# Performance work log

Measured on AMD Instinct MI355X. Metric: run time of the kernel, lower is better.

## Reference

```python
import jax, jax.numpy as jnp
import numpy as np

T, C, I, E = 8192, 512, 64, 32
NEG = -float(jnp.finfo(jnp.bfloat16).max)  # matches -torch.finfo(bfloat16).max in source


def _l2norm(x, axis):
    return x / jnp.maximum(jnp.linalg.norm(x, axis=axis, keepdims=True), 1e-12)


def setup_inputs() -> dict:
    key = jax.random.key(0)
    k1, k2, k3, k4 = jax.random.split(key, 4)
    hidden_states = jax.random.normal(k1, (T, C), dtype=jnp.float32)
    sim_matrix = jax.random.normal(k2, (C, E), dtype=jnp.float32)
    gates = jnp.zeros((E,), dtype=jnp.float32)
    # nn.Linear default init ~ U(-1/sqrt(fan_in), 1/sqrt(fan_in)); any scale works for a reference
    W1 = jax.random.uniform(k3, (E, C, I), dtype=jnp.float32, minval=-1, maxval=1) / np.sqrt(C)
    W2 = jax.random.uniform(k4, (E, I, C), dtype=jnp.float32, minval=-1, maxval=1) / np.sqrt(I)
    return {"hidden_states": hidden_states, "sim_matrix": sim_matrix, "gates": gates, "W1": W1, "W2": W2}


def reference(hidden_states, sim_matrix, gates, W1, W2):
    x = hidden_states
    # --- DynamicGate ---
    logits = _l2norm(x, -1) @ _l2norm(sim_matrix, 0)          # (T, E) cosine similarity
    pre_act_logits = logits - jax.nn.sigmoid(gates)            # (T, E)
    gated = jax.nn.relu(pre_act_logits)
    # STE: forward hard 0/1, backward identity
    ste_mask = gated + jax.lax.stop_gradient((gated > 0).astype(gated.dtype) - gated)
    inactive = jnp.sum(ste_mask > 0, axis=1) == 0              # tokens with no active expert
    k_fb = E // 2
    _, topk_idx = jax.lax.top_k(logits, k_fb)                  # (T, k_fb)
    onehot = jnp.zeros((T, E), dtype=bool).at[jnp.arange(T)[:, None], topk_idx].set(True)
    fb_pos = inactive[:, None] & onehot                        # positions force-set to 1.0
    activation_mask = jnp.where(fb_pos, jnp.float32(1.0), ste_mask)
    masked = jnp.where(activation_mask > 0, gated, NEG)
    routing_weights = jax.nn.softmax(masked, axis=-1)          # (T, E)
    # --- experts (dense equivalent of sort-dispatch; inactive pairs are zeroed,
    # matching the (T,E,C) zero tensor + index_put_ in the source) ---
    h = jax.nn.gelu(jnp.einsum('tc,eci->tei', x, W1), approximate=False)
    y = jnp.einsum('tei,eic->tec', h, W2)                      # (T, E, C)
    full_expert_outputs = y * jax.lax.stop_gradient(activation_mask)[:, :, None]
    final_output = jnp.einsum('te,tec->tc', routing_weights, full_expert_outputs)
    return final_output, full_expert_outputs, pre_act_logits, activation_mask
```

## Files before the change

kernel.cpp:

```cpp
#include <hip/hip_runtime.h>
#include <math.h>

#define T_ 8192
#define C_ 512
#define I_ 64
#define E_ 32

static constexpr float NEGMAX = -3.3895313892515355e+38f;

typedef float v4f __attribute__((ext_vector_type(4)));

static constexpr size_t WS_RW       = 0;
static constexpr size_t WS_SIMNORM  = (size_t)T_ * E_;
static constexpr size_t WS_MASKBITS = WS_SIMNORM + 64;
static constexpr size_t WS_ACOUNT   = WS_MASKBITS + T_;
static constexpr size_t WS_ALIST    = WS_ACOUNT + 64;

static constexpr size_t OUT_FINAL = 0;
static constexpr size_t OUT_FEO   = (size_t)T_ * C_;
static constexpr size_t OUT_PAL   = OUT_FEO + (size_t)T_ * E_ * C_;
static constexpr size_t OUT_AM    = OUT_PAL + (size_t)T_ * E_;

__global__ __launch_bounds__(256) void k_simnorm(const float* __restrict__ sim,
                                                 double* __restrict__ simnorm) {
  int e = threadIdx.x & 31, seg = threadIdx.x >> 5;
  double s = 0.0;
  for (int c = seg * 64; c < seg * 64 + 64; ++c) {
    double v = (double)sim[(size_t)c * E_ + e];
    s = fma(v, v, s);
  }
  __shared__ double red[8][32];
  red[seg][e] = s;
  __syncthreads();
  if (threadIdx.x < 32) {
    double tot = 0.0;
    for (int k = 0; k < 8; ++k) tot += red[k][threadIdx.x];
    simnorm[threadIdx.x] = sqrt(tot);
  }
}

__global__ __launch_bounds__(256) void k_gate(
    const float* __restrict__ x, const float* __restrict__ sim,
    const float* __restrict__ gates, const double* __restrict__ simnorm,
    float* __restrict__ pal, float* __restrict__ am,
    float* __restrict__ rw, unsigned* __restrict__ maskbits) {
  int lane = threadIdx.x & 63, wv = threadIdx.x >> 6;
  int t = blockIdx.x * 4 + wv;

  __shared__ float xr[4][512];
  const float* xp = x + (size_t)t * C_;
  v4f v0 = *(const v4f*)(xp + lane * 8);
  v4f v1 = *(const v4f*)(xp + lane * 8 + 4);
  *(v4f*)&xr[wv][lane * 8] = v0;
  *(v4f*)&xr[wv][lane * 8 + 4] = v1;
  double ss = (double)v0[0]*v0[0] + (double)v0[1]*v0[1]
            + (double)v0[2]*v0[2] + (double)v0[3]*v0[3]
            + (double)v1[0]*v1[0] + (double)v1[1]*v1[1]
            + (double)v1[2]*v1[2] + (double)v1[3]*v1[3];
  #pragma unroll
  for (int m = 1; m < 64; m <<= 1) ss += __shfl_xor(ss, m, 64);
  __syncthreads();

  int h = lane >> 5, e = lane & 31;
  const float* sp = sim + (size_t)(h * 256) * E_ + e;
  const float* xh = &xr[wv][h * 256];
  double acc = 0.0;
  #pragma unroll 8
  for (int c = 0; c < 256; ++c)
    acc = fma((double)xh[c], (double)sp[(size_t)c * E_], acc);
  acc += __shfl_xor(acc, 32, 64);

  double xn = sqrt(ss); if (xn < 1e-12) xn = 1e-12;
  double sn = simnorm[e]; if (sn < 1e-12) sn = 1e-12;
  float logit = (float)(acc / (xn * sn));
  float sg  = 1.f / (1.f + expf(-gates[e]));
  float pre = logit - sg;
  float gated = fmaxf(pre, 0.f);
  bool act = gated > 0.f;

  unsigned long long bal = __ballot(act);
  bool tok_inactive = ((unsigned)(bal & 0xffffffffull) == 0u);

  float mask;
  if (tok_inactive) {
    int rank = 0;
    #pragma unroll 1
    for (int j2 = 0; j2 < 32; ++j2) {
      float lj = __shfl(logit, j2, 32);
      if (lj > logit || (lj == logit && j2 < e)) ++rank;
    }
    mask = (rank < 16) ? 1.f : 0.f;
  } else {
    mask = act ? 1.f : 0.f;
  }

  float masked = (mask > 0.f) ? gated : NEGMAX;
  float mx = masked;
  #pragma unroll
  for (int m = 1; m < 32; m <<= 1) mx = fmaxf(mx, __shfl_xor(mx, m, 32));
  float ex = expf(masked - mx);
  float sum = ex;
  #pragma unroll
  for (int m = 1; m < 32; m <<= 1) sum += __shfl_xor(sum, m, 32);
  float w = ex / sum;

  unsigned mb = (unsigned)(__ballot(mask > 0.f) & 0xffffffffull);
  if (h == 0) {
    pal[(size_t)t * E_ + e] = pre;
    am [(size_t)t * E_ + e] = mask;
    rw [(size_t)t * E_ + e] = w;
    if (e == 0) maskbits[t] = mb;
  }
}

__global__ __launch_bounds__(1024) void k_lists(const unsigned* __restrict__ maskbits,
                                                unsigned* __restrict__ acount,
                                                unsigned* __restrict__ alist) {
  int e = blockIdx.x;
  int tid = threadIdx.x, lane = tid & 63, wv = tid >> 6;
  __shared__ unsigned wcnt[16], woff[16], stotal, sbase;
  if (tid == 0) sbase = 0;
  __syncthreads();
  for (int chunk = 0; chunk < 8; ++chunk) {
    int t = chunk * 1024 + tid;
    bool bit = (maskbits[t] >> e) & 1u;
    unsigned long long bal = __ballot(bit);
    unsigned prefix = (unsigned)__popcll(bal & ((1ull << lane) - 1ull));
    if (lane == 0) wcnt[wv] = (unsigned)__popcll(bal);
    __syncthreads();
    if (tid == 0) {
      unsigned r = 0;
      for (int k = 0; k < 16; ++k) { woff[k] = r; r += wcnt[k]; }
      stotal = r;
    }
    __syncthreads();
    if (bit) alist[(size_t)e * T_ + sbase + woff[wv] + prefix] = (unsigned)t;
    __syncthreads();
    if (tid == 0) sbase += stotal;
    __syncthreads();
  }
  if (tid == 0) acount[e] = sbase;
}

__global__ __launch_bounds__(256) void k_expert(
    const float* __restrict__ x, const float* __restrict__ W1,
    const float* __restrict__ W2, const unsigned* __restrict__ acount,
    const unsigned* __restrict__ alist, float* __restrict__ feo) {
  int bid = blockIdx.x;
  int xcd = bid & 7, j = bid >> 3;
  int e = xcd + 8 * (j & 3);
  int chunk = j >> 2;
  unsigned nact = acount[e];
  int start = chunk * 64;
  if ((unsigned)start >= nact) return;
  int nt = min(64, (int)nact - start);

  __shared__ __align__(16) char arena[51200];
  float (*xT)[68] = (float (*)[68])arena;
  float* w1t      = (float*)(arena + 17408);
  float* w2p      = (float*)arena;
  float (*hT)[68] = (float (*)[68])(arena + 33792);
  __shared__ int toks[64];

  int tid = threadIdx.x;
  if (tid < 64) {
    int idx = start + tid;
    toks[tid] = (int)alist[(size_t)e * T_ + ((idx < (int)nact) ? idx : start)];
  }
  __syncthreads();

  int ty = tid >> 4, tx = tid & 15;
  int tl = tid >> 2, m = tid & 3;
  const float* xrow = x + (size_t)toks[tl] * C_;

  float acc1[4][4];
  #pragma unroll
  for (int i = 0; i < 4; ++i)
    #pragma unroll
    for (int jj = 0; jj < 4; ++jj) acc1[i][jj] = 0.f;

  for (int kt = 0; kt < 8; ++kt) {
    const float* xp = xrow + kt * 64 + m * 16;
    #pragma unroll
    for (int q = 0; q < 4; ++q) {
      v4f v = *(const v4f*)(xp + q * 4);
      int kk = m * 16 + q * 4;
      xT[kk + 0][tl] = v[0];
      xT[kk + 1][tl] = v[1];
      xT[kk + 2][tl] = v[2];
      xT[kk + 3][tl] = v[3];
    }
    const float* wp = W1 + (size_t)e * C_ * I_ + (size_t)kt * 64 * I_;
    #pragma unroll
    for (int q = 0; q < 4; ++q) {
      int flat = q * 1024 + tid * 4;
      *(v4f*)(w1t + flat) = *(const v4f*)(wp + flat);
    }
    __syncthreads();
    #pragma unroll 4
    for (int kk = 0; kk < 64; ++kk) {
      v4f a = *(const v4f*)&xT[kk][ty * 4];
      v4f b = *(const v4f*)(w1t + kk * 64 + tx * 4);
      #pragma unroll
      for (int i = 0; i < 4; ++i)
        #pragma unroll
        for (int jj = 0; jj < 4; ++jj)
          acc1[i][jj] = fmaf(a[i], b[jj], acc1[i][jj]);
    }
    __syncthreads();
  }

  #pragma unroll
  for (int i = 0; i < 4; ++i)
    #pragma unroll
    for (int jj = 0; jj < 4; ++jj) {
      float v = acc1[i][jj];
      float g = 0.5f * v * (1.f + erff(v * 0.70710678118654752f));
      hT[tx * 4 + jj][ty * 4 + i] = g;
    }
  __syncthreads();

  for (int p = 0; p < 4; ++p) {
    const float* wp2 = W2 + (size_t)e * I_ * C_ + p * 128;
    #pragma unroll
    for (int q = 0; q < 8; ++q) {
      int flat = q * 1024 + tid * 4;
      int kk = flat >> 7, cc = flat & 127;
      *(v4f*)(w2p + flat) = *(const v4f*)(wp2 + (size_t)kk * C_ + cc);
    }
    __syncthreads();

    float accA[4][4], accB[4][4];
    #pragma unroll
    for (int i = 0; i < 4; ++i)
      #pragma unroll
      for (int jj = 0; jj < 4; ++jj) { accA[i][jj] = 0.f; accB[i][jj] = 0.f; }

    #pragma unroll 4
    for (int kk = 0; kk < 64; ++kk) {
      v4f a  = *(const v4f*)&hT[kk][ty * 4];
      v4f b0 = *(const v4f*)(w2p + kk * 128 + tx * 4);
      v4f b1 = *(const v4f*)(w2p + kk * 128 + 64 + tx * 4);
      #pragma unroll
      for (int i = 0; i < 4; ++i) {
        #pragma unroll
        for (int jj = 0; jj < 4; ++jj) {
          accA[i][jj] = fmaf(a[i], b0[jj], accA[i][jj]);
          accB[i][jj] = fmaf(a[i], b1[jj], accB[i][jj]);
        }
      }
    }

    #pragma unroll
    for (int i = 0; i < 4; ++i) {
      int tkn = ty * 4 + i;
      if (tkn < nt) {
        float* op = feo + ((size_t)toks[tkn] * E_ + e) * C_ + p * 128;
        v4f va = {accA[i][0], accA[i][1], accA[i][2], accA[i][3]};
        v4f vb = {accB[i][0], accB[i][1], accB[i][2], accB[i][3]};
        *(v4f*)(op + tx * 4)      = va;
        *(v4f*)(op + 64 + tx * 4) = vb;
      }
    }
    __syncthreads();
  }
}

__global__ __launch_bounds__(256) void k_final(float* __restrict__ feo,
                                               const float* __restrict__ rw,
                                               const unsigned* __restrict__ maskbits,
                                               float* __restrict__ fout) {
  int lane = threadIdx.x & 63, wv = threadIdx.x >> 6;
  int t = blockIdx.x * 4 + wv;
  unsigned bits = maskbits[t];
  float wlane = (lane < 32) ? rw[(size_t)t * E_ + lane] : 0.f;
  v4f acc0 = {0.f, 0.f, 0.f, 0.f};
  v4f acc1 = {0.f, 0.f, 0.f, 0.f};
  v4f zero = {0.f, 0.f, 0.f, 0.f};
  size_t rowbase = (size_t)t * E_ * C_;
  #pragma unroll 1
  for (int e = 0; e < E_; ++e) {
    float we = __shfl(wlane, e, 64);
    float* rp = feo + rowbase + (size_t)e * C_;
    if (bits & (1u << e)) {
      v4f f0 = *(const v4f*)(rp + lane * 4);
      v4f f1 = *(const v4f*)(rp + 256 + lane * 4);
      acc0 += we * f0;
      acc1 += we * f1;
    } else {
      *(v4f*)(rp + lane * 4)       = zero;
      *(v4f*)(rp + 256 + lane * 4) = zero;
    }
  }
  *(v4f*)(fout + (size_t)t * C_ + lane * 4)       = acc0;
  *(v4f*)(fout + (size_t)t * C_ + 256 + lane * 4) = acc1;
}

extern "C" void kernel_launch(void* const* d_in, const int* in_sizes, int n_in,
                              void* d_out, int out_size, void* d_ws, size_t ws_size,
                              hipStream_t stream) {
  const float* x     = (const float*)d_in[0];
  const float* sim   = (const float*)d_in[1];
  const float* gates = (const float*)d_in[2];
  const float* W1    = (const float*)d_in[3];
  const float* W2    = (const float*)d_in[4];
  float* out = (float*)d_out;
  float* ws  = (float*)d_ws;

  float*    rw       = ws + WS_RW;
  double*   simnorm  = (double*)(ws + WS_SIMNORM);
  unsigned* maskbits = (unsigned*)(ws + WS_MASKBITS);
  unsigned* acount   = (unsigned*)(ws + WS_ACOUNT);
  unsigned* alist    = (unsigned*)(ws + WS_ALIST);

  k_simnorm<<<1, 256, 0, stream>>>(sim, simnorm);
  k_gate<<<T_ / 4, 256, 0, stream>>>(x, sim, gates, simnorm,
                                     out + OUT_PAL, out + OUT_AM, rw, maskbits);
  k_lists<<<E_, 1024, 0, stream>>>(maskbits, acount, alist);
  k_expert<<<4096, 256, 0, stream>>>(x, W1, W2, acount, alist, out + OUT_FEO);
  k_final<<<T_ / 4, 256, 0, stream>>>(out + OUT_FEO, rw, maskbits, out + OUT_FINAL);
}
```

Baseline: 853.2 us.

## Use split-bf16 MFMA (3-term) for expert GEMMs instead of FP32 FMA

Rewrites the expert kernel's two GEMMs to use bf16 MFMA 16x16x32 instructions. Each fp32 operand is split into high and low bf16 parts and combined with three MFMAs, which keeps accuracy close to fp32. Operands are converted and staged into padded LDS tiles with a new layout. This trades extra conversion ALU work and scalar (non-vectorized) output stores for matrix-core throughput in place of scalar FMA loops.

```diff
diff --git a/kernel.cpp b/kernel.cpp
--- a/kernel.cpp
+++ b/kernel.cpp
@@ -9,6 +9,11 @@
 static constexpr float NEGMAX = -3.3895313892515355e+38f;
 
 typedef float v4f __attribute__((ext_vector_type(4)));
+typedef float f32x4 __attribute__((ext_vector_type(4)));
+typedef short s16x8 __attribute__((ext_vector_type(8)));
+typedef unsigned short u16;
+typedef unsigned short u16x4 __attribute__((ext_vector_type(4)));
+typedef unsigned short u16x8 __attribute__((ext_vector_type(8)));
 
 static constexpr size_t WS_RW       = 0;
 static constexpr size_t WS_SIMNORM  = (size_t)T_ * E_;
@@ -20,6 +25,16 @@
 static constexpr size_t OUT_FEO   = (size_t)T_ * C_;
 static constexpr size_t OUT_PAL   = OUT_FEO + (size_t)T_ * E_ * C_;
 static constexpr size_t OUT_AM    = OUT_PAL + (size_t)T_ * E_;
+
+__device__ inline u16 f2bf(float x) {
+  union { float f; unsigned u; } v; v.f = x;
+  unsigned r = v.u + 0x7fffu + ((v.u >> 16) & 1u);
+  return (u16)(r >> 16);
+}
+__device__ inline float bf2f(u16 h) {
+  union { unsigned u; float f; } v; v.u = ((unsigned)h) << 16;
+  return v.f;
+}
 
 __global__ __launch_bounds__(256) void k_simnorm(const float* __restrict__ sim,
                                                  double* __restrict__ simnorm) {
@@ -102,13 +117,13 @@
   float sum = ex;
   #pragma unroll
   for (int m = 1; m < 32; m <<= 1) sum += __shfl_xor(sum, m, 32);
-  float w = ex / sum;
+  float wgt = ex / sum;
 
   unsigned mb = (unsigned)(__ballot(mask > 0.f) & 0xffffffffull);
   if (h == 0) {
     pal[(size_t)t * E_ + e] = pre;
     am [(size_t)t * E_ + e] = mask;
-    rw [(size_t)t * E_ + e] = w;
+    rw [(size_t)t * E_ + e] = wgt;
     if (e == 0) maskbits[t] = mb;
   }
 }
@@ -140,6 +155,13 @@
     __syncthreads();
   }
   if (tid == 0) acount[e] = sbase;
+}
+
+__device__ inline f32x4 mfma3(s16x8 ah, s16x8 al, s16x8 bh, s16x8 bl, f32x4 c) {
+  c = __builtin_amdgcn_mfma_f32_16x16x32_bf16(ah, bh, c, 0, 0, 0);
+  c = __builtin_amdgcn_mfma_f32_16x16x32_bf16(ah, bl, c, 0, 0, 0);
+  c = __builtin_amdgcn_mfma_f32_16x16x32_bf16(al, bh, c, 0, 0, 0);
+  return c;
 }
 
 __global__ __launch_bounds__(256) void k_expert(
@@ -155,111 +177,152 @@
   if ((unsigned)start >= nact) return;
   int nt = min(64, (int)nact - start);
 
-  __shared__ __align__(16) char arena[51200];
-  float (*xT)[68] = (float (*)[68])arena;
-  float* w1t      = (float*)(arena + 17408);
-  float* w2p      = (float*)arena;
-  float (*hT)[68] = (float (*)[68])(arena + 33792);
+  __shared__ __align__(16) char arena[55296];
   __shared__ int toks[64];
+  u16* xs_h = (u16*)arena;
+  u16* xs_l = (u16*)(arena + 9216);
+  u16* w1_h = (u16*)(arena + 18432);
+  u16* w1_l = (u16*)(arena + 27648);
+  u16* gm_h = (u16*)arena;
+  u16* gm_l = (u16*)(arena + 9216);
+  u16* w2_h = (u16*)(arena + 18432);
+  u16* w2_l = (u16*)(arena + 36864);
 
   int tid = threadIdx.x;
+  int lane = tid & 63, w = tid >> 6;
+  int lr = lane & 15, lg = lane >> 4;
+
   if (tid < 64) {
     int idx = start + tid;
-    toks[tid] = (int)alist[(size_t)e * T_ + ((idx < (int)nact) ? idx : start)];
-  }
-  __syncthreads();
-
-  int ty = tid >> 4, tx = tid & 15;
-  int tl = tid >> 2, m = tid & 3;
-  const float* xrow = x + (size_t)toks[tl] * C_;
-
-  float acc1[4][4];
-  #pragma unroll
-  for (int i = 0; i < 4; ++i)
-    #pragma unroll
-    for (int jj = 0; jj < 4; ++jj) acc1[i][jj] = 0.f;
-
-  for (int kt = 0; kt < 8; ++kt) {
-    const float* xp = xrow + kt * 64 + m * 16;
-    #pragma unroll
-    for (int q = 0; q < 4; ++q) {
-      v4f v = *(const v4f*)(xp + q * 4);
-      int kk = m * 16 + q * 4;
-      xT[kk + 0][tl] = v[0];
-      xT[kk + 1][tl] = v[1];
-      xT[kk + 2][tl] = v[2];
-      xT[kk + 3][tl] = v[3];
-    }
-    const float* wp = W1 + (size_t)e * C_ * I_ + (size_t)kt * 64 * I_;
-    #pragma unroll
-    for (int q = 0; q < 4; ++q) {
-      int flat = q * 1024 + tid * 4;
-      *(v4f*)(w1t + flat) = *(const v4f*)(wp + flat);
-    }
-    __syncthreads();
-    #pragma unroll 4
-    for (int kk = 0; kk < 64; ++kk) {
-      v4f a = *(const v4f*)&xT[kk][ty * 4];
-      v4f b = *(const v4f*)(w1t + kk * 64 + tx * 4);
-      #pragma unroll
-      for (int i = 0; i < 4; ++i)
-        #pragma unroll
-        for (int jj = 0; jj < 4; ++jj)
-          acc1[i][jj] = fmaf(a[i], b[jj], acc1[i][jj]);
-    }
-    __syncthreads();
-  }
-
-  #pragma unroll
-  for (int i = 0; i < 4; ++i)
-    #pragma unroll
-    for (int jj = 0; jj < 4; ++jj) {
-      float v = acc1[i][jj];
+    toks[tid] = (int)alist[(size_t)e * T_ + (idx < (int)nact ? idx : start)];
+  }
+  __syncthreads();
+
+  f32x4 acc1[4];
+  #pragma unroll
+  for (int n = 0; n < 4; ++n) acc1[n] = (f32x4){0.f, 0.f, 0.f, 0.f};
+
+  int srow = tid >> 2, su = tid & 3;
+  int wiq = tid & 15, wc4 = tid >> 4;
+  const float* w1b = W1 + (size_t)e * C_ * I_;
+  const float* xrow = x + (size_t)toks[srow] * C_;
+
+  for (int kc = 0; kc < 8; ++kc) {
+    {
+      const float* src = xrow + kc * 64 + su * 16;
+      float f[16];
+      *(v4f*)(f)      = *(const v4f*)(src);
+      *(v4f*)(f + 4)  = *(const v4f*)(src + 4);
+      *(v4f*)(f + 8)  = *(const v4f*)(src + 8);
+      *(v4f*)(f + 12) = *(const v4f*)(src + 12);
+      u16 h[16], l[16];
+      #pragma unroll
+      for (int q = 0; q < 16; ++q) {
+        h[q] = f2bf(f[q]);
+        l[q] = f2bf(f[q] - bf2f(h[q]));
+      }
+      int off = srow * 72 + su * 16;
+      *(u16x8*)(xs_h + off)     = *(u16x8*)(h);
+      *(u16x8*)(xs_h + off + 8) = *(u16x8*)(h + 8);
+      *(u16x8*)(xs_l + off)     = *(u16x8*)(l);
+      *(u16x8*)(xs_l + off + 8) = *(u16x8*)(l + 8);
+    }
+    {
+      const float* src = w1b + (size_t)(kc * 64 + wc4 * 4) * I_ + wiq * 4;
+      v4f b0 = *(const v4f*)(src);
+      v4f b1 = *(const v4f*)(src + I_);
+      v4f b2 = *(const v4f*)(src + 2 * I_);
+      v4f b3 = *(const v4f*)(src + 3 * I_);
+      #pragma unroll
+      for (int ii = 0; ii < 4; ++ii) {
+        float c0 = b0[ii], c1 = b1[ii], c2 = b2[ii], c3 = b3[ii];
+        u16 h0 = f2bf(c0), h1 = f2bf(c1), h2 = f2bf(c2), h3 = f2bf(c3);
+        u16x4 hv = {h0, h1, h2, h3};
+        u16x4 lv = {f2bf(c0 - bf2f(h0)), f2bf(c1 - bf2f(h1)),
+                    f2bf(c2 - bf2f(h2)), f2bf(c3 - bf2f(h3))};
+        int off = (wiq * 4 + ii) * 72 + wc4 * 4;
+        *(u16x4*)(w1_h + off) = hv;
+        *(u16x4*)(w1_l + off) = lv;
+      }
+    }
+    __syncthreads();
+    #pragma unroll
+    for (int s = 0; s < 2; ++s) {
+      int ko = s * 32 + lg * 8;
+      s16x8 ah = *(const s16x8*)(xs_h + (w * 16 + lr) * 72 + ko);
+      s16x8 al = *(const s16x8*)(xs_l + (w * 16 + lr) * 72 + ko);
+      #pragma unroll
+      for (int n = 0; n < 4; ++n) {
+        s16x8 bh = *(const s16x8*)(w1_h + (n * 16 + lr) * 72 + ko);
+        s16x8 bl = *(const s16x8*)(w1_l + (n * 16 + lr) * 72 + ko);
+        acc1[n] = mfma3(ah, al, bh, bl, acc1[n]);
+      }
+    }
+    __syncthreads();
+  }
+
+  #pragma unroll
+  for (int n = 0; n < 4; ++n) {
+    #pragma unroll
+    for (int r = 0; r < 4; ++r) {
+      float v = acc1[n][r];
       float g = 0.5f * v * (1.f + erff(v * 0.70710678118654752f));
-      hT[tx * 4 + jj][ty * 4 + i] = g;
-    }
-  __syncthreads();
-
+      u16 h = f2bf(g);
+      int off = (w * 16 + lg * 4 + r) * 72 + n * 16 + lr;
+      gm_h[off] = h;
+      gm_l[off] = f2bf(g - bf2f(h));
+    }
+  }
+  __syncthreads();
+
+  const float* w2b = W2 + (size_t)e * I_ * C_;
   for (int p = 0; p < 4; ++p) {
-    const float* wp2 = W2 + (size_t)e * I_ * C_ + p * 128;
-    #pragma unroll
-    for (int q = 0; q < 8; ++q) {
-      int flat = q * 1024 + tid * 4;
-      int kk = flat >> 7, cc = flat & 127;
-      *(v4f*)(w2p + flat) = *(const v4f*)(wp2 + (size_t)kk * C_ + cc);
-    }
-    __syncthreads();
-
-    float accA[4][4], accB[4][4];
-    #pragma unroll
-    for (int i = 0; i < 4; ++i)
-      #pragma unroll
-      for (int jj = 0; jj < 4; ++jj) { accA[i][jj] = 0.f; accB[i][jj] = 0.f; }
-
-    #pragma unroll 4
-    for (int kk = 0; kk < 64; ++kk) {
-      v4f a  = *(const v4f*)&hT[kk][ty * 4];
-      v4f b0 = *(const v4f*)(w2p + kk * 128 + tx * 4);
-      v4f b1 = *(const v4f*)(w2p + kk * 128 + 64 + tx * 4);
-      #pragma unroll
-      for (int i = 0; i < 4; ++i) {
-        #pragma unroll
-        for (int jj = 0; jj < 4; ++jj) {
-          accA[i][jj] = fmaf(a[i], b0[jj], accA[i][jj]);
-          accB[i][jj] = fmaf(a[i], b1[jj], accB[i][jj]);
+    #pragma unroll
+    for (int task = tid; task < 512; task += 256) {
+      int cq = task >> 4, iq = task & 15;
+      const float* src = w2b + (size_t)(iq * 4) * C_ + p * 128 + cq * 4;
+      v4f b0 = *(const v4f*)(src);
+      v4f b1 = *(const v4f*)(src + C_);
+      v4f b2 = *(const v4f*)(src + 2 * C_);
+      v4f b3 = *(const v4f*)(src + 3 * C_);
+      #pragma unroll
+      for (int cc = 0; cc < 4; ++cc) {
+        float c0 = b0[cc], c1 = b1[cc], c2 = b2[cc], c3 = b3[cc];
+        u16 h0 = f2bf(c0), h1 = f2bf(c1), h2 = f2bf(c2), h3 = f2bf(c3);
+        u16x4 hv = {h0, h1, h2, h3};
+        u16x4 lv = {f2bf(c0 - bf2f(h0)), f2bf(c1 - bf2f(h1)),
+                    f2bf(c2 - bf2f(h2)), f2bf(c3 - bf2f(h3))};
+        int off = (cq * 4 + cc) * 72 + iq * 4;
+        *(u16x4*)(w2_h + off) = hv;
+        *(u16x4*)(w2_l + off) = lv;
+      }
+    }
+    __syncthreads();
+
+    f32x4 acc2[8];
+    #pragma unroll
+    for (int n = 0; n < 8; ++n) acc2[n] = (f32x4){0.f, 0.f, 0.f, 0.f};
+    #pragma unroll
+    for (int s = 0; s < 2; ++s) {
+      int ko = s * 32 + lg * 8;
+      s16x8 ah = *(const s16x8*)(gm_h + (w * 16 + lr) * 72 + ko);
+      s16x8 al = *(const s16x8*)(gm_l + (w * 16 + lr) * 72 + ko);
+      #pragma unroll
+      for (int n = 0; n < 8; ++n) {
+        s16x8 bh = *(const s16x8*)(w2_h + (n * 16 + lr) * 72 + ko);
+        s16x8 bl = *(const s16x8*)(w2_l + (n * 16 + lr) * 72 + ko);
+        acc2[n] = mfma3(ah, al, bh, bl, acc2[n]);
+      }
+    }
+    #pragma unroll
+    for (int n = 0; n < 8; ++n) {
+      #pragma unroll
+      for (int r = 0; r < 4; ++r) {
+        int slot = w * 16 + lg * 4 + r;
+        if (slot < nt) {
+          feo[((size_t)toks[slot] * E_ + e) * C_ + p * 128 + n * 16 + lr] =
+              acc2[n][r];
         }
-      }
-    }
-
-    #pragma unroll
-    for (int i = 0; i < 4; ++i) {
-      int tkn = ty * 4 + i;
-      if (tkn < nt) {
-        float* op = feo + ((size_t)toks[tkn] * E_ + e) * C_ + p * 128;
-        v4f va = {accA[i][0], accA[i][1], accA[i][2], accA[i][3]};
-        v4f vb = {accB[i][0], accB[i][1], accB[i][2], accB[i][3]};
-        *(v4f*)(op + tx * 4)      = va;
-        *(v4f*)(op + 64 + tx * 4) = vb;
       }
     }
     __syncthreads();
```

Result: no change. 844.7 us (-1.0%).
